# Kernel tuning notes

Measured on AMD Instinct MI355X. Metric: run time of the kernel, lower is better.

Reference implementation:

```python
import jax, jax.numpy as jnp
import numpy as np

N_NODES = 50000
K = 16            # fixed node degree (regular graph -> reshapeable edge list)
N_FEAT = 128
N_TEMPL = 16
M_TEMPL = 8
ALPHA = 0.5       # FGW structure/feature trade-off


def setup_inputs() -> dict:
    key = jax.random.key(0)
    k1, k2, k3, k4 = jax.random.split(key, 4)
    x = jax.random.normal(k1, (N_NODES, N_FEAT), dtype=jnp.float32)
    # fixed-degree graph: node i has exactly K neighbors -> edge_index[1] reshapes to [N, K]
    dst = jax.random.randint(k2, (N_NODES * K,), 0, N_NODES)
    src = jnp.repeat(jnp.arange(N_NODES), K)
    edge_index = jnp.stack([src, dst])  # [2, N*K]
    templates = jax.random.uniform(k3, (N_TEMPL, M_TEMPL, M_TEMPL), dtype=jnp.float32)
    templates_features = jax.random.uniform(k4, (N_TEMPL, M_TEMPL, N_FEAT), dtype=jnp.float32)
    return {"x": x, "edge_index": edge_index,
            "templates": templates, "templates_features": templates_features}


def reference(x, edge_index, templates, templates_features):
    """LTFWG forward: per-node FGW distance between the node's 1-hop induced
    subgraph (neighbor features + induced adjacency) and each learned template,
    evaluated under the uniform product coupling (closed form). Output [N, T]."""
    n = x.shape[0]
    nbrs = edge_index[1].reshape(n, K)               # [N,K] neighbor ids per node
    f = x[nbrs]                                      # [N,K,F] gathered neighbor features

    # ---- feature (Wasserstein) term: E_a||f_a||^2 + E_c||Ft_c||^2 - 2<E_a f_a, E_c Ft_c>
    sq = jnp.mean(jnp.sum(f * f, axis=-1), axis=-1)                 # [N]
    fmean = jnp.mean(f, axis=1)                                     # [N,F]
    tsq = jnp.mean(jnp.sum(templates_features ** 2, axis=-1), -1)   # [T]
    tmean = jnp.mean(templates_features, axis=1)                    # [T,F]
    feat = sq[:, None] + tsq[None, :] - 2.0 * (fmean @ tmean.T)     # [N,T]

    # ---- structure (Gromov) term with induced adjacency among the K neighbors
    non = nbrs[nbrs]                                  # [N,K,K] neighbors-of-neighbors
    # C[n,a,b] = 1 iff nbrs[n,b] is a neighbor of nbrs[n,a]
    C = jnp.any(non[:, :, :, None] == nbrs[:, None, None, :], axis=2).astype(x.dtype)
    mC = jnp.mean(C, axis=(1, 2))                     # [N]; C binary -> mean(C^2)=mean(C)
    mCt = jnp.mean(templates, axis=(1, 2))            # [T]
    mCt2 = jnp.mean(templates ** 2, axis=(1, 2))      # [T]
    struct = mC[:, None] + mCt2[None, :] - 2.0 * mC[:, None] * mCt[None, :]  # [N,T]

    return (1.0 - ALPHA) * feat + ALPHA * struct
```

## Files before the change

kernel.cpp:

```cpp
#include <hip/hip_runtime.h>
#include <stdint.h>

#define N_NODES 50000
#define KDEG    16
#define NFEAT   128
#define NTPL    16
#define MTPL    8
#define NTILES  ((N_NODES + 63) / 64)

#define TMEAN_OFF 0
#define TSQ_OFF   2048
#define MCT_OFF   2064
#define MCT2_OFF  2080
#define Z_OFF     2112
#define WS_FLOATS (Z_OFF + N_NODES * NTPL)
#define WS_BYTES  ((size_t)WS_FLOATS * 4)

template<int CTRL>
__device__ __forceinline__ float dpp_addf(float v) {
    int t = __builtin_amdgcn_update_dpp(0, __float_as_int(v), CTRL, 0xF, 0xF, 1);
    return v + __int_as_float(t);
}
template<int CTRL>
__device__ __forceinline__ int dpp_addi(int v) {
    int t = __builtin_amdgcn_update_dpp(0, v, CTRL, 0xF, 0xF, 1);
    return v + t;
}
#define ROR1 0x121
#define ROR2 0x122
#define ROR4 0x124
#define ROR8 0x128
#define QPX1 0xB1
#define QPX2 0x4E

__device__ __forceinline__ float row16_sum(float v) {
    v = dpp_addf<ROR1>(v);
    v = dpp_addf<ROR2>(v);
    v = dpp_addf<ROR4>(v);
    v = dpp_addf<ROR8>(v);
    return v;
}
__device__ __forceinline__ int row16_sumi(int v) {
    v = dpp_addi<ROR1>(v);
    v = dpp_addi<ROR2>(v);
    v = dpp_addi<ROR4>(v);
    v = dpp_addi<ROR8>(v);
    return v;
}
__device__ __forceinline__ float quad_sum(float v) {
    v = dpp_addf<QPX1>(v);
    v = dpp_addf<QPX2>(v);
    return v;
}

__global__ __launch_bounds__(256, 4)
void ltfwg_zbuild(const float* __restrict__ x,
                  const float* __restrict__ tmpl,
                  const float* __restrict__ tfeat,
                  float* __restrict__ ws) {
    const int tid = threadIdx.x;

    __shared__ float tm_lds[NTPL * 144];

    {
        const int f  = tid & 127;
        const int t0 = (tid >> 7) * 8;
        #pragma unroll
        for (int k = 0; k < 8; ++k) {
            int t = t0 + k;
            float s = 0.f;
            #pragma unroll
            for (int m = 0; m < MTPL; ++m)
                s += tfeat[t * (MTPL * NFEAT) + m * NFEAT + f];
            tm_lds[t * 144 + (f >> 5) * 36 + (f & 31)] = s * 0.125f;
        }
    }

    if (blockIdx.x == 0) {
        const int t = tid >> 4;
        const int j = tid & 15;
        float ssq = 0.f;
        #pragma unroll
        for (int m = 0; m < MTPL; ++m)
            #pragma unroll
            for (int c = 0; c < 8; ++c) {
                float v = tfeat[t * (MTPL * NFEAT) + m * NFEAT + j * 8 + c];
                ssq += v * v;
            }
        float sv = 0.f, sv2 = 0.f;
        #pragma unroll
        for (int c = 0; c < 4; ++c) {
            float v = tmpl[t * 64 + j * 4 + c];
            sv += v;
            sv2 += v * v;
        }
        ssq = row16_sum(ssq);
        sv  = row16_sum(sv);
        sv2 = row16_sum(sv2);
        if (j == 0) {
            ws[TSQ_OFF + t]  = ssq * 0.125f;
            ws[MCT_OFF + t]  = sv  * (1.f / 64.f);
            ws[MCT2_OFF + t] = sv2 * (1.f / 64.f);
        }
    }
    __syncthreads();

    const int q  = tid & 3;
    const int rr = tid >> 2;
    for (int tile = blockIdx.x; tile < NTILES; tile += gridDim.x) {
        int n = tile * 64 + rr;
        if (n < N_NODES) {
            const float4* x4 = (const float4*)x + (size_t)n * 32 + q * 8;
            float4 xv[8];
            #pragma unroll
            for (int jj = 0; jj < 8; ++jj) xv[jj] = x4[jj];

            float s2 = 0.f;
            #pragma unroll
            for (int jj = 0; jj < 8; ++jj)
                s2 += xv[jj].x * xv[jj].x + xv[jj].y * xv[jj].y +
                      xv[jj].z * xv[jj].z + xv[jj].w * xv[jj].w;

            float acc[NTPL];
            #pragma unroll
            for (int t = 0; t < NTPL; ++t) {
                const float* tb = tm_lds + t * 144 + q * 36;
                float a = 0.f;
                #pragma unroll
                for (int jj = 0; jj < 8; ++jj) {
                    float4 tv = *(const float4*)(tb + 4 * jj);
                    a += xv[jj].x * tv.x + xv[jj].y * tv.y +
                         xv[jj].z * tv.z + xv[jj].w * tv.w;
                }
                acc[t] = a;
            }

            float h = quad_sum(s2) * 0.5f;
            #pragma unroll
            for (int t = 0; t < NTPL; ++t) acc[t] = quad_sum(acc[t]);

            float b0, b1, b2, b3;
            if (q == 0)      { b0 = acc[0];  b1 = acc[1];  b2 = acc[2];  b3 = acc[3];  }
            else if (q == 1) { b0 = acc[4];  b1 = acc[5];  b2 = acc[6];  b3 = acc[7];  }
            else if (q == 2) { b0 = acc[8];  b1 = acc[9];  b2 = acc[10]; b3 = acc[11]; }
            else             { b0 = acc[12]; b1 = acc[13]; b2 = acc[14]; b3 = acc[15]; }
            ((float4*)(ws + Z_OFF))[(size_t)n * 4 + q] =
                make_float4(h - b0, h - b1, h - b2, h - b3);
        }
    }
}

__global__ __launch_bounds__(256, 8)
void ltfwg_gather(const int* __restrict__ dst, const float* __restrict__ ws,
                  float* __restrict__ out) {
    const int lane   = threadIdx.x & 63;
    const int gwave  = (blockIdx.x * blockDim.x + threadIdx.x) >> 6;
    const int nwaves = (gridDim.x * blockDim.x) >> 6;
    const int a = lane & 15;
    const int c = lane >> 4;

    const int tl = c * 4 + (lane & 3);
    const float A  = 0.5f * (ws[TSQ_OFF + tl] + ws[MCT2_OFF + tl]);
    const float Bc = 0.5f - ws[MCT_OFF + tl];
    const bool writer = (lane & 15) < 4;
    const float4* z4 = (const float4*)(ws + Z_OFF);
    const int4*  d4 = (const int4*)dst;

    int n = gwave;
    int nbr = (n < N_NODES) ? dst[n * KDEG + a] : 0;
    while (n < N_NODES) {
        const int n2 = n + nwaves;
        int nbr_next = (n2 < N_NODES) ? dst[n2 * KDEG + a] : 0;

        float4 v  = z4[(size_t)nbr * 4 + c];
        int4   cv = d4[(size_t)nbr * 4 + c];

        uint32_t m = 0;
        #pragma unroll
        for (int b = 0; b < KDEG; ++b) {
            int vb = __builtin_amdgcn_readlane(nbr, b);
            uint32_t hit = (uint32_t)((cv.x == vb) | (cv.y == vb) |
                                      (cv.z == vb) | (cv.w == vb));
            m |= hit << b;
        }
        m |= (uint32_t)__shfl_xor((int)m, 16);
        m |= (uint32_t)__shfl_xor((int)m, 32);
        int cm = row16_sumi(__popc(m));

        float v0 = row16_sum(v.x);
        float v1 = row16_sum(v.y);
        float v2 = row16_sum(v.z);
        float v3 = row16_sum(v.w);

        if (writer) {
            int j = lane & 3;
            float dsel = (j == 0) ? v0 : (j == 1) ? v1 : (j == 2) ? v2 : v3;
            float val = 0.0625f * dsel + A + (float)cm * (1.f / 256.f) * Bc;
            out[n * NTPL + tl] = val;
        }
        n = n2;
        nbr = nbr_next;
    }
}

__global__ void ltfwg_prep(const float* __restrict__ tmpl,
                           const float* __restrict__ tfeat,
                           float* __restrict__ ws) {
    const int t   = blockIdx.x;
    const int tid = threadIdx.x;
    float s = 0.f, ssq = 0.f;
    #pragma unroll
    for (int m = 0; m < MTPL; ++m) {
        float v = tfeat[t * (MTPL * NFEAT) + m * NFEAT + tid];
        s += v;
        ssq += v * v;
    }
    ws[TMEAN_OFF + t * NFEAT + tid] = s * 0.125f;
    __shared__ float red[128];
    red[tid] = ssq;
    __syncthreads();
    for (int o = 64; o > 0; o >>= 1) {
        if (tid < o) red[tid] += red[tid + o];
        __syncthreads();
    }
    if (tid == 0) ws[TSQ_OFF + t] = red[0] * 0.125f;
    if (tid < 64) {
        float v = tmpl[t * 64 + tid];
        float sv = v, sv2 = v * v;
        #pragma unroll
        for (int off = 32; off >= 1; off >>= 1) {
            sv  += __shfl_xor(sv, off);
            sv2 += __shfl_xor(sv2, off);
        }
        if (tid == 0) {
            ws[MCT_OFF + t]  = sv  * (1.f / 64.f);
            ws[MCT2_OFF + t] = sv2 * (1.f / 64.f);
        }
    }
}

__global__ __launch_bounds__(256, 4)
void ltfwg_fallback(const float* __restrict__ x, const int* __restrict__ dst,
                    const float* __restrict__ ws, float* __restrict__ out) {
    const int lane   = threadIdx.x & 63;
    const int wave   = (blockIdx.x * blockDim.x + threadIdx.x) >> 6;
    const int nwaves = (gridDim.x * blockDim.x) >> 6;
    float tm0[NTPL], tm1[NTPL];
    #pragma unroll
    for (int t = 0; t < NTPL; ++t) {
        float2 tv = ((const float2*)(ws + TMEAN_OFF + t * NFEAT))[lane];
        tm0[t] = tv.x;
        tm1[t] = tv.y;
    }
    const int tl = lane & 15;
    const float A  = 0.5f * (ws[TSQ_OFF + tl] + ws[MCT2_OFF + tl]);
    const float Bc = 0.5f - ws[MCT_OFF + tl];
    for (int n = wave; n < N_NODES; n += nwaves) {
        const int nbr = dst[n * KDEG + (lane & 15)];
        float fs0 = 0.f, fs1 = 0.f, sqa = 0.f;
        #pragma unroll
        for (int aa = 0; aa < KDEG; ++aa) {
            int nid = __shfl(nbr, aa);
            float2 fv = ((const float2*)x)[nid * (NFEAT / 2) + lane];
            fs0 += fv.x; fs1 += fv.y;
            sqa += fv.x * fv.x + fv.y * fv.y;
        }
        float dotp[NTPL];
        #pragma unroll
        for (int t = 0; t < NTPL; ++t) dotp[t] = fs0 * tm0[t] + fs1 * tm1[t];
        int nida = __shfl(nbr, lane >> 2);
        int4 cv = ((const int4*)(dst + nida * KDEG))[lane & 3];
        uint32_t m = 0;
        #pragma unroll
        for (int b = 0; b < KDEG; ++b) {
            int vb = __shfl(nbr, b);
            uint32_t hit = (uint32_t)((cv.x == vb) | (cv.y == vb) |
                                      (cv.z == vb) | (cv.w == vb));
            m |= hit << b;
        }
        m |= (uint32_t)__shfl_xor((int)m, 1);
        m |= (uint32_t)__shfl_xor((int)m, 2);
        float cnt = (float)__popc(m);
        #pragma unroll
        for (int off = 32; off >= 1; off >>= 1) {
            sqa += __shfl_xor(sqa, off);
            cnt += __shfl_xor(cnt, off);
            #pragma unroll
            for (int t = 0; t < NTPL; ++t) dotp[t] += __shfl_xor(dotp[t], off);
        }
        float dsel = dotp[0];
        #pragma unroll
        for (int t = 1; t < NTPL; ++t) dsel = (lane == t) ? dotp[t] : dsel;
        if (lane < NTPL) {
            float mC = cnt * (1.0f / 1024.0f);
            out[n * NTPL + lane] = 0.03125f * sqa - 0.0625f * dsel + A + mC * Bc;
        }
    }
}

extern "C" void kernel_launch(void* const* d_in, const int* in_sizes, int n_in,
                              void* d_out, int out_size, void* d_ws, size_t ws_size,
                              hipStream_t stream) {
    const float* x     = (const float*)d_in[0];
    const int*   edge  = (const int*)d_in[1];
    const float* tmpl  = (const float*)d_in[2];
    const float* tfeat = (const float*)d_in[3];
    float* ws  = (float*)d_ws;
    float* out = (float*)d_out;
    const int* dst = edge + (N_NODES * KDEG);

    if (ws_size >= WS_BYTES) {
        ltfwg_zbuild<<<NTILES, 256, 0, stream>>>(x, tmpl, tfeat, ws);
        ltfwg_gather<<<2048, 256, 0, stream>>>(dst, ws, out);
    } else {
        ltfwg_prep<<<NTPL, 128, 0, stream>>>(tmpl, tfeat, ws);
        ltfwg_fallback<<<1024, 256, 0, stream>>>(x, dst, ws, out);
    }
}
```

Before: 103.2 us.

## Interleave per-node Z values with neighbor lists and software-pipeline the gather

The zbuild kernel now writes each node's 16 Z values together with its 16 neighbor ids into one 128-byte row of the workspace. The gather then fetches both with a single random-access row instead of hitting two separate arrays. The gather loop also gains one more stage of prefetch, issuing the next node's Z and neighbor loads before processing the current node, to hide random-access latency. The costs are twice the workspace footprint, extra zbuild write traffic and higher register pressure in the gather.

```diff
diff --git a/kernel.cpp b/kernel.cpp
--- a/kernel.cpp
+++ b/kernel.cpp
@@ -13,7 +13,8 @@
 #define MCT_OFF   2064
 #define MCT2_OFF  2080
 #define Z_OFF     2112
-#define WS_FLOATS (Z_OFF + N_NODES * NTPL)
+#define ZROW      32
+#define WS_FLOATS (Z_OFF + N_NODES * ZROW)
 #define WS_BYTES  ((size_t)WS_FLOATS * 4)
 
 template<int CTRL>
@@ -55,6 +56,7 @@
 
 __global__ __launch_bounds__(256, 4)
 void ltfwg_zbuild(const float* __restrict__ x,
+                  const int*   __restrict__ dst,
                   const float* __restrict__ tmpl,
                   const float* __restrict__ tfeat,
                   float* __restrict__ ws) {
@@ -107,6 +109,7 @@
 
     const int q  = tid & 3;
     const int rr = tid >> 2;
+    const int4* d4 = (const int4*)dst;
     for (int tile = blockIdx.x; tile < NTILES; tile += gridDim.x) {
         int n = tile * 64 + rr;
         if (n < N_NODES) {
@@ -114,6 +117,7 @@
             float4 xv[8];
             #pragma unroll
             for (int jj = 0; jj < 8; ++jj) xv[jj] = x4[jj];
+            int4 dv = d4[(size_t)n * 4 + q];
 
             float s2 = 0.f;
             #pragma unroll
@@ -144,8 +148,9 @@
             else if (q == 1) { b0 = acc[4];  b1 = acc[5];  b2 = acc[6];  b3 = acc[7];  }
             else if (q == 2) { b0 = acc[8];  b1 = acc[9];  b2 = acc[10]; b3 = acc[11]; }
             else             { b0 = acc[12]; b1 = acc[13]; b2 = acc[14]; b3 = acc[15]; }
-            ((float4*)(ws + Z_OFF))[(size_t)n * 4 + q] =
-                make_float4(h - b0, h - b1, h - b2, h - b3);
+            float4* rw = (float4*)(ws + Z_OFF) + (size_t)n * 8;
+            rw[q] = make_float4(h - b0, h - b1, h - b2, h - b3);
+            ((int4*)rw)[4 + q] = dv;
         }
     }
 }
@@ -163,43 +168,55 @@
     const float A  = 0.5f * (ws[TSQ_OFF + tl] + ws[MCT2_OFF + tl]);
     const float Bc = 0.5f - ws[MCT_OFF + tl];
     const bool writer = (lane & 15) < 4;
-    const float4* z4 = (const float4*)(ws + Z_OFF);
-    const int4*  d4 = (const int4*)dst;
-
-    int n = gwave;
-    int nbr = (n < N_NODES) ? dst[n * KDEG + a] : 0;
-    while (n < N_NODES) {
-        const int n2 = n + nwaves;
-        int nbr_next = (n2 < N_NODES) ? dst[n2 * KDEG + a] : 0;
-
-        float4 v  = z4[(size_t)nbr * 4 + c];
-        int4   cv = d4[(size_t)nbr * 4 + c];
+    const float4* rz = (const float4*)(ws + Z_OFF);
+    const int4*   rd = (const int4*)(ws + Z_OFF);
+
+    int n0 = gwave;
+    int nbr0 = (n0 < N_NODES) ? dst[n0 * KDEG + a] : 0;
+    float4 v0  = make_float4(0.f, 0.f, 0.f, 0.f);
+    int4   cv0 = make_int4(0, 0, 0, 0);
+    if (n0 < N_NODES) {
+        v0  = rz[(size_t)nbr0 * 8 + c];
+        cv0 = rd[(size_t)nbr0 * 8 + 4 + c];
+    }
+    int n1 = n0 + nwaves;
+    int nbr1 = (n1 < N_NODES) ? dst[n1 * KDEG + a] : 0;
+
+    while (n0 < N_NODES) {
+        float4 v1  = make_float4(0.f, 0.f, 0.f, 0.f);
+        int4   cv1 = make_int4(0, 0, 0, 0);
+        if (n1 < N_NODES) {
+            v1  = rz[(size_t)nbr1 * 8 + c];
+            cv1 = rd[(size_t)nbr1 * 8 + 4 + c];
+        }
+        const int n2 = n1 + nwaves;
+        int nbr2 = (n2 < N_NODES) ? dst[n2 * KDEG + a] : 0;
 
         uint32_t m = 0;
         #pragma unroll
         for (int b = 0; b < KDEG; ++b) {
-            int vb = __builtin_amdgcn_readlane(nbr, b);
-            uint32_t hit = (uint32_t)((cv.x == vb) | (cv.y == vb) |
-                                      (cv.z == vb) | (cv.w == vb));
+            int vb = __builtin_amdgcn_readlane(nbr0, b);
+            uint32_t hit = (uint32_t)((cv0.x == vb) | (cv0.y == vb) |
+                                      (cv0.z == vb) | (cv0.w == vb));
             m |= hit << b;
         }
         m |= (uint32_t)__shfl_xor((int)m, 16);
         m |= (uint32_t)__shfl_xor((int)m, 32);
         int cm = row16_sumi(__popc(m));
 
-        float v0 = row16_sum(v.x);
-        float v1 = row16_sum(v.y);
-        float v2 = row16_sum(v.z);
-        float v3 = row16_sum(v.w);
+        float s0 = row16_sum(v0.x);
+        float s1 = row16_sum(v0.y);
+        float s2 = row16_sum(v0.z);
+        float s3 = row16_sum(v0.w);
 
         if (writer) {
             int j = lane & 3;
-            float dsel = (j == 0) ? v0 : (j == 1) ? v1 : (j == 2) ? v2 : v3;
-            float val = 0.0625f * dsel + A + (float)cm * (1.f / 256.f) * Bc;
-            out[n * NTPL + tl] = val;
-        }
-        n = n2;
-        nbr = nbr_next;
+            float dsel = (j == 0) ? s0 : (j == 1) ? s1 : (j == 2) ? s2 : s3;
+            out[n0 * NTPL + tl] = 0.0625f * dsel + A + (float)cm * (1.f / 256.f) * Bc;
+        }
+
+        n0 = n1; nbr0 = nbr1; v0 = v1; cv0 = cv1;
+        n1 = n2; nbr1 = nbr2;
     }
 }
 
@@ -310,7 +327,7 @@
     const int* dst = edge + (N_NODES * KDEG);
 
     if (ws_size >= WS_BYTES) {
-        ltfwg_zbuild<<<NTILES, 256, 0, stream>>>(x, tmpl, tfeat, ws);
+        ltfwg_zbuild<<<NTILES, 256, 0, stream>>>(x, dst, tmpl, tfeat, ws);
         ltfwg_gather<<<2048, 256, 0, stream>>>(dst, ws, out);
     } else {
         ltfwg_prep<<<NTPL, 128, 0, stream>>>(tmpl, tfeat, ws);
```

New measurement: 103.6 us, median of 2. No clear change (+0.4%).
